# Optimization experiments

Measured on AMD Instinct MI355X. Metric: run time of the kernel, lower is better.

## Reference

```python
import jax, jax.numpy as jnp
import numpy as np


def log_g(x):
    # log of g(x) = where(x>=0, x+0.5, sigmoid(x)) in log space
    return jnp.where(x >= 0, jnp.log(jax.nn.relu(x) + 0.5), -jax.nn.softplus(-x))


def setup_inputs() -> dict:
    key = jax.random.key(0)
    k1, k2, k3 = jax.random.split(key, 3)
    B, S, D = 4, 4096, 2048
    D_INNER = int(D * 1.5)  # 3072
    x = jax.random.normal(k1, (B, S, D), dtype=jnp.float32)
    w_hg = jax.random.normal(k2, (D, 2 * D_INNER), dtype=jnp.float32) * (D ** -0.5)
    w_out = jax.random.normal(k3, (D_INNER, D), dtype=jnp.float32) * (D_INNER ** -0.5)
    return {"x": x, "w_hg": w_hg, "w_out": w_out}


def reference(x, w_hg, w_out):
    # x: [B,S,D]; w_hg: [D, 2*Di]; w_out: [Di, D]
    hg = jnp.einsum('bsd,de->bse', x, w_hg)
    hidden, gate = jnp.split(hg, 2, axis=-1)  # each [B,S,Di]
    log_coeffs = -jax.nn.softplus(gate)        # log(1 - z)
    log_z = -jax.nn.softplus(-gate)            # log z
    log_values = log_z + log_g(hidden)
    # Heinsen associative scan in log space along seq axis
    a_star = jnp.cumsum(log_coeffs, axis=1)
    log_h = a_star + jax.lax.cumlogsumexp(log_values - a_star, axis=1)
    h = jnp.exp(log_h)                         # [B,S,Di]
    out = jnp.einsum('bse,ed->bsd', h, w_out)  # to_out Linear (expansion != 1)
    return out
```

## Files before the change

### kernel.cpp

```cpp
#include <hip/hip_runtime.h>
#include <hip/hip_bf16.h>
#include <stdint.h>

typedef __hip_bfloat16 bf16;
typedef __attribute__((ext_vector_type(8))) short short8;
typedef __attribute__((ext_vector_type(4))) float floatx4;
typedef __attribute__((address_space(3))) const unsigned short lu16;

__device__ __forceinline__ unsigned short f2bu(float f) {
  bf16 b = __float2bfloat16(f);
  return *reinterpret_cast<unsigned short*>(&b);
}

__device__ __forceinline__ void stf(float* p, float v) { *p = v; }
__device__ __forceinline__ void stf(bf16* p, float v) { *p = __float2bfloat16(v); }

__device__ __forceinline__ void ld4(const bf16* p, float* o) {
  ushort4 v = *(const ushort4*)p;
  o[0] = __bfloat162float(*(bf16*)&v.x);
  o[1] = __bfloat162float(*(bf16*)&v.y);
  o[2] = __bfloat162float(*(bf16*)&v.z);
  o[3] = __bfloat162float(*(bf16*)&v.w);
}

__device__ __forceinline__ void gl_lds16(const bf16* g, bf16* l) {
  __builtin_amdgcn_global_load_lds((const __attribute__((address_space(1))) void*)g,
                                   (__attribute__((address_space(3))) void*)l,
                                   16, 0, 0);
}

template <int OFF>
__device__ __forceinline__ short8 ldsro(lu16* p) {
  short8 r;
  asm volatile("ds_read_b128 %0, %1 offset:%2" : "=v"(r) : "v"(p), "i"(OFF));
  return r;
}

#define BAR() __builtin_amdgcn_s_barrier()
#define LGKM0() do { asm volatile("s_waitcnt lgkmcnt(0)" ::: "memory"); \
                     __builtin_amdgcn_sched_barrier(0); } while (0)
#define VMCNT(n) asm volatile("s_waitcnt vmcnt(" #n ")" ::: "memory")

__global__ void cvt_f32_bf16(const float* __restrict__ in, bf16* __restrict__ out, long n4) {
  long i = (long)blockIdx.x * blockDim.x + threadIdx.x;
  if (i >= n4) return;
  float4 v = ((const float4*)in)[i];
  ushort4 o;
  o.x = f2bu(v.x); o.y = f2bu(v.y); o.z = f2bu(v.z); o.w = f2bu(v.w);
  ((ushort4*)out)[i] = o;
}

__global__ void transpose_f32_to_bf16(const float* __restrict__ in, bf16* __restrict__ out,
                                      int R, int Cc) {
  __shared__ float tile[32][33];
  int tx = threadIdx.x & 31;
  int ty = threadIdx.x >> 5;
  int c0 = blockIdx.x * 32;
  int r0 = blockIdx.y * 32;
#pragma unroll
  for (int i = 0; i < 32; i += 8)
    tile[ty + i][tx] = in[(long)(r0 + ty + i) * Cc + c0 + tx];
  __syncthreads();
#pragma unroll
  for (int i = 0; i < 32; i += 8)
    out[(long)(c0 + ty + i) * R + r0 + tx] = __float2bfloat16(tile[tx][ty + i]);
}

template <typename OUT_T>
__global__ __launch_bounds__(512, 2) void gemm256(const bf16* __restrict__ A,
                                                  const bf16* __restrict__ BT,
                                                  OUT_T* __restrict__ C,
                                                  int M, int N, int K) {
  __shared__ __align__(16) bf16 lds[2][2][256][64];

  const int tid = threadIdx.x;
  const int w = tid >> 6;
  const int lane = tid & 63;
  const int quad = lane >> 4;
  const int r16 = lane & 15;
  const int wm = (w >> 2) * 128;
  const int wn = (w & 3) * 64;

  const int nbx = N >> 8;
  const int nwg = nbx * (M >> 8);
  const int bid = blockIdx.x;
  const int swz = (bid & 7) * (nwg >> 3) + (bid >> 3);
  const long bM = (long)(swz / nbx) * 256;
  const long bN = (long)(swz % nbx) * 256;

  const int r0 = tid >> 3;
  const int c8 = (tid & 7) ^ (r0 & 7);
  const bf16* Ag = A + (bM + r0) * (long)K + c8 * 8;
  const bf16* Bg = BT + (bN + r0) * (long)K + c8 * 8;
  const int lslot = w * 512;

  bf16* Am0 = &lds[0][0][0][0];
  bf16* Am1 = &lds[1][0][0][0];
  bf16* Bm0 = &lds[0][1][0][0];
  bf16* Bm1 = &lds[1][1][0][0];

  auto stage = [&](const bf16* g, bf16* lmat, int half, int kt) {
    const bf16* gs = g + (long)half * 128 * K + (long)kt * 64;
    bf16* ls = lmat + half * 8192 + lslot;
    gl_lds16(gs, ls);
    gl_lds16(gs + 64L * K, ls + 4096);
  };

  const int lofsA = (wm + r16) * 64;
  const int lofsB = (wn + r16) * 64;
  const int c8x0 = ((0 * 4 + quad) ^ (r16 & 7)) * 8;
  const int c8x1 = ((1 * 4 + quad) ^ (r16 & 7)) * 8;
  lu16* lb = (lu16*)&lds[0][0][0][0];
  lu16* pA0k0 = lb + 0 * 32768 + 0 * 16384 + lofsA + c8x0;
  lu16* pA0k1 = lb + 0 * 32768 + 0 * 16384 + lofsA + c8x1;
  lu16* pA1k0 = lb + 1 * 32768 + 0 * 16384 + lofsA + c8x0;
  lu16* pA1k1 = lb + 1 * 32768 + 0 * 16384 + lofsA + c8x1;
  lu16* pB0k0 = lb + 0 * 32768 + 1 * 16384 + lofsB + c8x0;
  lu16* pB0k1 = lb + 0 * 32768 + 1 * 16384 + lofsB + c8x1;
  lu16* pB1k0 = lb + 1 * 32768 + 1 * 16384 + lofsB + c8x0;
  lu16* pB1k1 = lb + 1 * 32768 + 1 * 16384 + lofsB + c8x1;

  floatx4 acc[8][4];
#pragma unroll
  for (int a = 0; a < 8; a++)
#pragma unroll
    for (int b = 0; b < 4; b++) acc[a][b] = (floatx4){0.f, 0.f, 0.f, 0.f};

  short8 af[4][2], bq0[2][2], bq1[2][2];

#define READ_A(P0, P1, MG) do { \
  af[0][0] = ldsro<((MG)*4 + 0) * 2048>(P0); af[0][1] = ldsro<((MG)*4 + 0) * 2048>(P1); \
  af[1][0] = ldsro<((MG)*4 + 1) * 2048>(P0); af[1][1] = ldsro<((MG)*4 + 1) * 2048>(P1); \
  af[2][0] = ldsro<((MG)*4 + 2) * 2048>(P0); af[2][1] = ldsro<((MG)*4 + 2) * 2048>(P1); \
  af[3][0] = ldsro<((MG)*4 + 3) * 2048>(P0); af[3][1] = ldsro<((MG)*4 + 3) * 2048>(P1); \
} while (0)

#define READ_B(P0, P1, NG, BQ) do { \
  BQ[0][0] = ldsro<((NG)*2 + 0) * 2048>(P0); BQ[0][1] = ldsro<((NG)*2 + 0) * 2048>(P1); \
  BQ[1][0] = ldsro<((NG)*2 + 1) * 2048>(P0); BQ[1][1] = ldsro<((NG)*2 + 1) * 2048>(P1); \
} while (0)

#define PH_MMA(MG, NG, BQ) do { \
  __builtin_amdgcn_s_setprio(1); \
  _Pragma("unroll") \
  for (int mf = 0; mf < 4; ++mf) \
    _Pragma("unroll") \
    for (int nf = 0; nf < 2; ++nf) { \
      acc[(MG)*4 + mf][(NG)*2 + nf] = __builtin_amdgcn_mfma_f32_16x16x32_bf16( \
          af[mf][0], BQ[nf][0], acc[(MG)*4 + mf][(NG)*2 + nf], 0, 0, 0); \
      acc[(MG)*4 + mf][(NG)*2 + nf] = __builtin_amdgcn_mfma_f32_16x16x32_bf16( \
          af[mf][1], BQ[nf][1], acc[(MG)*4 + mf][(NG)*2 + nf], 0, 0, 0); \
    } \
  __builtin_amdgcn_s_setprio(0); \
} while (0)

#define KTILE(PA0, PA1, PB0, PB1, S1, S3, S4a, S4b, VMX) do { \
  READ_A(PA0, PA1, 0); READ_B(PB0, PB1, 0, bq0); S1; \
  BAR(); LGKM0(); PH_MMA(0, 0, bq0); BAR(); \
  READ_B(PB0, PB1, 1, bq1); \
  BAR(); LGKM0(); PH_MMA(0, 1, bq1); BAR(); \
  READ_A(PA0, PA1, 1); S3; \
  BAR(); LGKM0(); PH_MMA(1, 1, bq1); BAR(); \
  S4a; S4b; BAR(); PH_MMA(1, 0, bq0); VMX; BAR(); \
} while (0)

  stage(Ag, Am0, 0, 0); stage(Ag, Am0, 1, 0);
  stage(Bg, Bm0, 0, 0); stage(Bg, Bm0, 1, 0);
  stage(Bg, Bm1, 0, 1);
  stage(Bg, Bm1, 1, 1); stage(Ag, Am1, 0, 1);
  VMCNT(6);
  BAR();

  const int NI = K >> 7;
  for (int i = 0; i < NI - 1; ++i) {
    const int k1 = 2 * i + 1, k2 = 2 * i + 2, k3 = 2 * i + 3;
    KTILE(pA0k0, pA0k1, pB0k0, pB0k1,
          stage(Ag, Am1, 1, k1),
          stage(Bg, Bm0, 0, k2),
          stage(Bg, Bm0, 1, k2), stage(Ag, Am0, 0, k2), VMCNT(6));
    KTILE(pA1k0, pA1k1, pB1k0, pB1k1,
          stage(Ag, Am0, 1, k2),
          stage(Bg, Bm1, 0, k3),
          stage(Bg, Bm1, 1, k3), stage(Ag, Am1, 0, k3), VMCNT(6));
  }
  {
    const int kl = 2 * NI - 1;
    KTILE(pA0k0, pA0k1, pB0k0, pB0k1,
          stage(Ag, Am1, 1, kl),
          (void)0, (void)0, (void)0, VMCNT(0));
    KTILE(pA1k0, pA1k1, pB1k0, pB1k1,
          (void)0, (void)0, (void)0, (void)0, (void)0);
  }

#undef KTILE
#undef PH_MMA
#undef READ_B
#undef READ_A

#pragma unroll
  for (int mf = 0; mf < 8; ++mf) {
#pragma unroll
    for (int i2 = 0; i2 < 4; ++i2) {
      long row = bM + wm + mf * 16 + quad * 4 + i2;
      OUT_T* crow = C + row * (long)N + bN + wn + r16;
#pragma unroll
      for (int nf = 0; nf < 4; ++nf) stf(&crow[nf * 16], acc[mf][nf][i2]);
    }
  }
}

__device__ __forceinline__ void cv_compute(float hval, float gval, float& c, float& v) {
  float eg = __expf(gval);
  c = 1.f / (1.f + eg);
  float z = 1.f - c;
  float gx = (hval >= 0.f) ? (hval + 0.5f) : (1.f / (1.f + __expf(-hval)));
  v = z * gx;
}

__global__ void scan_pass1(const bf16* __restrict__ hg, float* __restrict__ P,
                           float* __restrict__ V, int S, int Di, int NN, int nch) {
  int tid = blockIdx.x * blockDim.x + threadIdx.x;
  int De = Di >> 2;
  int e = (tid % De) * 4;
  int rest = tid / De;
  int ch = rest % nch;
  int b = rest / nch;
  int CH = S / nch;
  const bf16* ph = hg + ((long)(b * S + ch * CH)) * NN + e;
  float Pv[4] = {1.f, 1.f, 1.f, 1.f}, Vv[4] = {0.f, 0.f, 0.f, 0.f};
  for (int t = 0; t < CH; t++) {
    float hv[4], gv[4];
    ld4(ph, hv);
    ld4(ph + Di, gv);
#pragma unroll
    for (int j = 0; j < 4; j++) {
      float c, v;
      cv_compute(hv[j], gv[j], c, v);
      Pv[j] *= c;
      Vv[j] = fmaf(c, Vv[j], v);
    }
    ph += NN;
  }
  long base = ((long)(b * nch + ch)) * Di + e;
  *(float4*)&P[base] = make_float4(Pv[0], Pv[1], Pv[2], Pv[3]);
  *(float4*)&V[base] = make_float4(Vv[0], Vv[1], Vv[2], Vv[3]);
}

__global__ void scan_pass2(const float* __restrict__ P, const float* __restrict__ V,
                           float* __restrict__ Hc, int Di, int nch) {
  int tid = blockIdx.x * blockDim.x + threadIdx.x;
  int e = tid % Di;
  int b = tid / Di;
  float H = 0.f;
  for (int j = 0; j < nch; j++) {
    long idx = ((long)(b * nch + j)) * Di + e;
    Hc[idx] = H;
    H = fmaf(P[idx], H, V[idx]);
  }
}

__global__ void scan_pass3(const bf16* __restrict__ hg, const float* __restrict__ Hc,
                           bf16* __restrict__ h, int S, int Di, int NN, int nch) {
  int tid = blockIdx.x * blockDim.x + threadIdx.x;
  int De = Di >> 2;
  int e = (tid % De) * 4;
  int rest = tid / De;
  int ch = rest % nch;
  int b = rest / nch;
  int CH = S / nch;
  const bf16* ph = hg + ((long)(b * S + ch * CH)) * NN + e;
  bf16* po = h + ((long)(b * S + ch * CH)) * Di + e;
  long base = ((long)(b * nch + ch)) * Di + e;
  float4 hc = *(const float4*)&Hc[base];
  float H[4] = {hc.x, hc.y, hc.z, hc.w};
  for (int t = 0; t < CH; t++) {
    float hv[4], gv[4];
    ld4(ph, hv);
    ld4(ph + Di, gv);
    ushort4 o;
#pragma unroll
    for (int j = 0; j < 4; j++) {
      float c, v;
      cv_compute(hv[j], gv[j], c, v);
      H[j] = fmaf(c, H[j], v);
    }
    o.x = f2bu(H[0]); o.y = f2bu(H[1]); o.z = f2bu(H[2]); o.w = f2bu(H[3]);
    *(ushort4*)po = o;
    ph += NN;
    po += Di;
  }
}

extern "C" void kernel_launch(void* const* d_in, const int* in_sizes, int n_in,
                              void* d_out, int out_size, void* d_ws, size_t ws_size,
                              hipStream_t stream) {
  const int B = 4, S = 4096, D = 2048, Di = 3072, NN = 6144;
  const int Mr = B * S;
  const int NCH = 64;

  const float* x = (const float*)d_in[0];
  const float* w_hg = (const float*)d_in[1];
  const float* w_out = (const float*)d_in[2];
  float* out = (float*)d_out;

  char* wp = (char*)d_ws;
  bf16* x_bf = (bf16*)wp;  wp += (size_t)Mr * D * 2;
  bf16* whgT = (bf16*)wp;  wp += (size_t)NN * D * 2;
  bf16* woutT = (bf16*)wp; wp += (size_t)D * Di * 2;
  bf16* h_bf = (bf16*)wp;  wp += (size_t)Mr * Di * 2;
  bf16* hg = (bf16*)wp;    wp += (size_t)Mr * NN * 2;

  float* P = (float*)x_bf;
  float* V = P + (size_t)B * NCH * Di;
  float* Hc = V + (size_t)B * NCH * Di;

  cvt_f32_bf16<<<(int)(((long)Mr * D / 4 + 255) / 256), 256, 0, stream>>>(x, x_bf, (long)Mr * D / 4);
  transpose_f32_to_bf16<<<dim3(NN / 32, D / 32), 256, 0, stream>>>(w_hg, whgT, D, NN);
  transpose_f32_to_bf16<<<dim3(D / 32, Di / 32), 256, 0, stream>>>(w_out, woutT, Di, D);

  const int nwg1 = (NN / 256) * (Mr / 256);
  const int nwg2 = (D / 256) * (Mr / 256);
  int scan_vthreads = B * NCH * (Di / 4);

  gemm256<bf16><<<nwg1, 512, 0, stream>>>(x_bf, whgT, hg, Mr, NN, D);
  scan_pass1<<<scan_vthreads / 256, 256, 0, stream>>>(hg, P, V, S, Di, NN, NCH);
  scan_pass2<<<(B * Di) / 256, 256, 0, stream>>>(P, V, Hc, Di, NCH);
  scan_pass3<<<scan_vthreads / 256, 256, 0, stream>>>(hg, Hc, h_bf, S, Di, NN, NCH);

  gemm256<float><<<nwg2, 512, 0, stream>>>(h_bf, woutT, out, Mr, D, Di);
}
```

Before: 951.7 us.

## Overlap LDS fragment reads with MFMA via partial lgkmcnt waits

Restructures the GEMM k-tile inner schedule so LDS reads for A and B fragments are issued up front and MFMA groups start as soon as their operands arrive, using graded lgkmcnt waits instead of a full drain before each phase. It also removes the extra barrier pairs around each phase and reshuffles the global-to-LDS staging so each phase issues two stage calls, adjusting the vmcnt wait count to match. This targets LDS latency stalls between phases, but the staging reorder changes which A tile is prefetched in the prologue and could introduce LDS hazards.

```diff
diff --git a/kernel.cpp b/kernel.cpp
--- a/kernel.cpp
+++ b/kernel.cpp
@@ -37,8 +37,8 @@
 }
 
 #define BAR() __builtin_amdgcn_s_barrier()
-#define LGKM0() do { asm volatile("s_waitcnt lgkmcnt(0)" ::: "memory"); \
-                     __builtin_amdgcn_sched_barrier(0); } while (0)
+#define WAITLG(n) do { asm volatile("s_waitcnt lgkmcnt(" #n ")" ::: "memory"); \
+                       __builtin_amdgcn_sched_barrier(0); } while (0)
 #define VMCNT(n) asm volatile("s_waitcnt vmcnt(" #n ")" ::: "memory")
 
 __global__ void cvt_f32_bf16(const float* __restrict__ in, bf16* __restrict__ out, long n4) {
@@ -128,74 +128,90 @@
 
   short8 af[4][2], bq0[2][2], bq1[2][2];
 
-#define READ_A(P0, P1, MG) do { \
-  af[0][0] = ldsro<((MG)*4 + 0) * 2048>(P0); af[0][1] = ldsro<((MG)*4 + 0) * 2048>(P1); \
-  af[1][0] = ldsro<((MG)*4 + 1) * 2048>(P0); af[1][1] = ldsro<((MG)*4 + 1) * 2048>(P1); \
-  af[2][0] = ldsro<((MG)*4 + 2) * 2048>(P0); af[2][1] = ldsro<((MG)*4 + 2) * 2048>(P1); \
-  af[3][0] = ldsro<((MG)*4 + 3) * 2048>(P0); af[3][1] = ldsro<((MG)*4 + 3) * 2048>(P1); \
+#define MMAG(AR, MF, NB, BQ) do { \
+  acc[AR][NB]     = __builtin_amdgcn_mfma_f32_16x16x32_bf16(af[MF][0], BQ[0][0], acc[AR][NB], 0, 0, 0); \
+  acc[AR][NB]     = __builtin_amdgcn_mfma_f32_16x16x32_bf16(af[MF][1], BQ[0][1], acc[AR][NB], 0, 0, 0); \
+  acc[AR][NB + 1] = __builtin_amdgcn_mfma_f32_16x16x32_bf16(af[MF][0], BQ[1][0], acc[AR][NB + 1], 0, 0, 0); \
+  acc[AR][NB + 1] = __builtin_amdgcn_mfma_f32_16x16x32_bf16(af[MF][1], BQ[1][1], acc[AR][NB + 1], 0, 0, 0); \
 } while (0)
 
-#define READ_B(P0, P1, NG, BQ) do { \
-  BQ[0][0] = ldsro<((NG)*2 + 0) * 2048>(P0); BQ[0][1] = ldsro<((NG)*2 + 0) * 2048>(P1); \
-  BQ[1][0] = ldsro<((NG)*2 + 1) * 2048>(P0); BQ[1][1] = ldsro<((NG)*2 + 1) * 2048>(P1); \
+#define ISSUE_P1(PA0, PA1, PB0, PB1) do { \
+  af[0][0] = ldsro<0>(PA0);     af[0][1] = ldsro<0>(PA1); \
+  bq0[0][0] = ldsro<0>(PB0);    bq0[0][1] = ldsro<0>(PB1); \
+  bq0[1][0] = ldsro<2048>(PB0); bq0[1][1] = ldsro<2048>(PB1); \
+  af[1][0] = ldsro<2048>(PA0);  af[1][1] = ldsro<2048>(PA1); \
+  af[2][0] = ldsro<4096>(PA0);  af[2][1] = ldsro<4096>(PA1); \
+  af[3][0] = ldsro<6144>(PA0);  af[3][1] = ldsro<6144>(PA1); \
+  bq1[0][0] = ldsro<4096>(PB0); bq1[0][1] = ldsro<4096>(PB1); \
+  bq1[1][0] = ldsro<6144>(PB0); bq1[1][1] = ldsro<6144>(PB1); \
 } while (0)
 
-#define PH_MMA(MG, NG, BQ) do { \
+#define ISSUE_P3(PA0, PA1) do { \
+  af[0][0] = ldsro<8192>(PA0);  af[0][1] = ldsro<8192>(PA1); \
+  af[1][0] = ldsro<10240>(PA0); af[1][1] = ldsro<10240>(PA1); \
+  af[2][0] = ldsro<12288>(PA0); af[2][1] = ldsro<12288>(PA1); \
+  af[3][0] = ldsro<14336>(PA0); af[3][1] = ldsro<14336>(PA1); \
+} while (0)
+
+#define KTILE(PA0, PA1, PB0, PB1, S1, S2, S3, S4, VMX) do { \
+   \
+  ISSUE_P1(PA0, PA1, PB0, PB1); S1; \
   __builtin_amdgcn_s_setprio(1); \
-  _Pragma("unroll") \
-  for (int mf = 0; mf < 4; ++mf) \
-    _Pragma("unroll") \
-    for (int nf = 0; nf < 2; ++nf) { \
-      acc[(MG)*4 + mf][(NG)*2 + nf] = __builtin_amdgcn_mfma_f32_16x16x32_bf16( \
-          af[mf][0], BQ[nf][0], acc[(MG)*4 + mf][(NG)*2 + nf], 0, 0, 0); \
-      acc[(MG)*4 + mf][(NG)*2 + nf] = __builtin_amdgcn_mfma_f32_16x16x32_bf16( \
-          af[mf][1], BQ[nf][1], acc[(MG)*4 + mf][(NG)*2 + nf], 0, 0, 0); \
-    } \
+  WAITLG(10); MMAG(0, 0, 0, bq0); \
+  WAITLG(8);  MMAG(1, 1, 0, bq0); \
+  WAITLG(6);  MMAG(2, 2, 0, bq0); \
+  WAITLG(4);  MMAG(3, 3, 0, bq0); \
+  __builtin_amdgcn_s_setprio(0); BAR(); \
+   \
+  S2; WAITLG(0); \
+  __builtin_amdgcn_s_setprio(1); \
+  MMAG(0, 0, 2, bq1); MMAG(1, 1, 2, bq1); MMAG(2, 2, 2, bq1); MMAG(3, 3, 2, bq1); \
+  __builtin_amdgcn_s_setprio(0); BAR(); \
+   \
+  ISSUE_P3(PA0, PA1); S3; \
+  __builtin_amdgcn_s_setprio(1); \
+  WAITLG(6); MMAG(4, 0, 2, bq1); \
+  WAITLG(4); MMAG(5, 1, 2, bq1); \
+  WAITLG(2); MMAG(6, 2, 2, bq1); \
+  WAITLG(0); MMAG(7, 3, 2, bq1); \
+  __builtin_amdgcn_s_setprio(0); BAR(); \
+   \
+  S4; \
+  __builtin_amdgcn_s_setprio(1); \
+  MMAG(4, 0, 0, bq0); MMAG(5, 1, 0, bq0); MMAG(6, 2, 0, bq0); MMAG(7, 3, 0, bq0); \
   __builtin_amdgcn_s_setprio(0); \
-} while (0)
-
-#define KTILE(PA0, PA1, PB0, PB1, S1, S3, S4a, S4b, VMX) do { \
-  READ_A(PA0, PA1, 0); READ_B(PB0, PB1, 0, bq0); S1; \
-  BAR(); LGKM0(); PH_MMA(0, 0, bq0); BAR(); \
-  READ_B(PB0, PB1, 1, bq1); \
-  BAR(); LGKM0(); PH_MMA(0, 1, bq1); BAR(); \
-  READ_A(PA0, PA1, 1); S3; \
-  BAR(); LGKM0(); PH_MMA(1, 1, bq1); BAR(); \
-  S4a; S4b; BAR(); PH_MMA(1, 0, bq0); VMX; BAR(); \
+  VMX; BAR(); \
 } while (0)
 
   stage(Ag, Am0, 0, 0); stage(Ag, Am0, 1, 0);
   stage(Bg, Bm0, 0, 0); stage(Bg, Bm0, 1, 0);
-  stage(Bg, Bm1, 0, 1);
-  stage(Bg, Bm1, 1, 1); stage(Ag, Am1, 0, 1);
-  VMCNT(6);
+  stage(Bg, Bm1, 0, 1); stage(Bg, Bm1, 1, 1);
+  VMCNT(4);
   BAR();
 
   const int NI = K >> 7;
   for (int i = 0; i < NI - 1; ++i) {
     const int k1 = 2 * i + 1, k2 = 2 * i + 2, k3 = 2 * i + 3;
     KTILE(pA0k0, pA0k1, pB0k0, pB0k1,
-          stage(Ag, Am1, 1, k1),
-          stage(Bg, Bm0, 0, k2),
-          stage(Bg, Bm0, 1, k2), stage(Ag, Am0, 0, k2), VMCNT(6));
+          stage(Ag, Am1, 0, k1), stage(Ag, Am1, 1, k1),
+          stage(Bg, Bm0, 0, k2), stage(Bg, Bm0, 1, k2), VMCNT(4));
     KTILE(pA1k0, pA1k1, pB1k0, pB1k1,
-          stage(Ag, Am0, 1, k2),
-          stage(Bg, Bm1, 0, k3),
-          stage(Bg, Bm1, 1, k3), stage(Ag, Am1, 0, k3), VMCNT(6));
+          stage(Ag, Am0, 0, k2), stage(Ag, Am0, 1, k2),
+          stage(Bg, Bm1, 0, k3), stage(Bg, Bm1, 1, k3), VMCNT(4));
   }
   {
     const int kl = 2 * NI - 1;
     KTILE(pA0k0, pA0k1, pB0k0, pB0k1,
-          stage(Ag, Am1, 1, kl),
-          (void)0, (void)0, (void)0, VMCNT(0));
+          stage(Ag, Am1, 0, kl), stage(Ag, Am1, 1, kl),
+          (void)0, (void)0, VMCNT(0));
     KTILE(pA1k0, pA1k1, pB1k0, pB1k1,
           (void)0, (void)0, (void)0, (void)0, (void)0);
   }
 
 #undef KTILE
-#undef PH_MMA
-#undef READ_B
-#undef READ_A
+#undef ISSUE_P3
+#undef ISSUE_P1
+#undef MMAG
 
 #pragma unroll
   for (int mf = 0; mf < 8; ++mf) {
```

Result: no change. 936.2 us (-1.6%).
